# Kernel optimization log

Measured on AMD Instinct MI355X. Metric: run time of the kernel, lower is better.

## Reference

```python
import jax, jax.numpy as jnp
import numpy as np

B, S, D = 4, 2048, 1024
NEG_INF = jnp.float32(-jnp.inf)


def setup_inputs() -> dict:
    key = jax.random.key(0)
    kx, kq, kk, kv = jax.random.split(key, 4)
    scale = 0.02
    return {
        "x": jax.random.normal(kx, (B, S, D), dtype=jnp.float32),
        "Wq": jax.random.normal(kq, (D, D), dtype=jnp.float32) * scale,
        "Wk": jax.random.normal(kk, (D, D), dtype=jnp.float32) * scale,
        "Wv": jax.random.normal(kv, (D, D), dtype=jnp.float32) * scale,
    }


def reference(x, Wq, Wk, Wv):
    # nn.Linear(d_in, d_out): y = x @ W.T (no bias; qkv_bias=False)
    q = jnp.einsum("bsd,ed->bse", x, Wq)
    k = jnp.einsum("bsd,ed->bse", x, Wk)
    v = jnp.einsum("bsd,ed->bse", x, Wv)
    n = x.shape[1]
    scores = jnp.einsum("bqe,bke->bqk", q, k)  # [B, S, S]
    # causal mask: positions k > q are masked with -inf
    causal = jnp.tril(jnp.ones((n, n), dtype=bool))
    scores = jnp.where(causal[None, :, :], scores, NEG_INF)
    attn = jax.nn.softmax(scores / jnp.sqrt(jnp.float32(k.shape[-1])), axis=-1)
    # dropout p=0.0 (eval) -> identity
    return jnp.einsum("bqk,bke->bqe", attn, v)
```

## Files before the change

kernel.cpp:

```cpp
#include <hip/hip_runtime.h>
#include <hip/hip_bf16.h>
#include <stdint.h>
#include <stddef.h>


typedef __hip_bfloat16 bf16;
typedef short short8 __attribute__((ext_vector_type(8)));
typedef short short4v __attribute__((ext_vector_type(4)));
typedef float f32x4 __attribute__((ext_vector_type(4)));

#define BM 128
#define BN 128
#define BK 64
#define MSZ 8192
#define DD 1024

__device__ __forceinline__ void cstore(float* p, float v) { *p = v; }
__device__ __forceinline__ void cstore(bf16* p, float v) { *p = __float2bfloat16(v); }

__global__ __launch_bounds__(256)
void f2b(const float* __restrict__ s, bf16* __restrict__ d, int n) {
  const int i = (blockIdx.x * 256 + threadIdx.x) * 4;
  if (i >= n) return;
  const float4 v = *(const float4*)(s + i);
  bf16 t[4] = {__float2bfloat16(v.x), __float2bfloat16(v.y),
               __float2bfloat16(v.z), __float2bfloat16(v.w)};
  *(short4v*)(d + i) = *(short4v*)t;
}

__global__ __launch_bounds__(256)
void f2b3(const float* __restrict__ a, const float* __restrict__ b,
          const float* __restrict__ c, bf16* __restrict__ d, int n) {
  const float* s = (blockIdx.y == 0) ? a : (blockIdx.y == 1) ? b : c;
  const int i = (blockIdx.x * 256 + threadIdx.x) * 4;
  if (i >= n) return;
  const float4 v = *(const float4*)(s + i);
  bf16 t[4] = {__float2bfloat16(v.x), __float2bfloat16(v.y),
               __float2bfloat16(v.z), __float2bfloat16(v.w)};
  *(short4v*)(d + (size_t)blockIdx.y * n + i) = *(short4v*)t;
}

template <int MODE, typename CT>
__global__ __launch_bounds__(256, 3)
void gemm_bt(const bf16* __restrict__ A, const bf16* __restrict__ B,
             CT* __restrict__ C, bf16* __restrict__ C2,
             int lda, int ldb, int ldc, int K,
             long sA, long sB, long sC, float scale) {
  int by, bx;
  if (MODE == 2) {
    const int t = blockIdx.x;
    by = (int)((__fsqrt_rn(8.f * (float)t + 1.f) - 1.f) * 0.5f);
    while ((by + 1) * (by + 2) / 2 <= t) by++;
    while (by * (by + 1) / 2 > t) by--;
    bx = t - by * (by + 1) / 2;
  } else if (MODE == 3) {
    by = gridDim.y - 1 - blockIdx.y;
    bx = blockIdx.x;
  } else {
    by = blockIdx.y;
    bx = blockIdx.x;
  }

  __shared__ short8 As[8 * 128];
  __shared__ short8 Bs[8 * 128];

  const int tid = threadIdx.x;
  const int wave = tid >> 6, lane = tid & 63;
  const int wm = wave >> 1, wn = wave & 1;
  const int l15 = lane & 15, q4 = lane >> 4;
  const int bm0 = by * BM, bn0 = bx * BN;

  const bf16* Az = A + (long)blockIdx.z * sA;
  const bf16* Bz = B + (long)blockIdx.z * sB;
  CT* Cz = C + (long)blockIdx.z * sC;

  const int kg = (lane >> 3) & 7;
  const int rl = wave * 8 + (lane & 7);

  const bf16* apg = Az + (size_t)(bm0 + rl) * lda + kg * 8;
  const bf16* bpg = Bz + (size_t)(bn0 + rl) * ldb + kg * 8;
  const size_t la32 = (size_t)32 * lda, lb32 = (size_t)32 * ldb;
  short8* dstA = &As[kg * 128 + rl];
  short8* dstB = &Bs[kg * 128 + rl];

  const int Ke = (MODE == 3) ? min(K, (by + 1) * BM) : K;

  f32x4 acc[4][4] = {};
  short8 ra[4], rb[4];

#pragma unroll
  for (int j = 0; j < 4; j++) {
    ra[j] = *(const short8*)(apg + j * la32);
    rb[j] = *(const short8*)(bpg + j * lb32);
  }

  for (int k0 = 0; k0 < Ke; k0 += BK) {
    __syncthreads();
#pragma unroll
    for (int j = 0; j < 4; j++) {
      dstA[j * 32] = ra[j];
      dstB[j * 32] = rb[j];
    }
    __syncthreads();

    const int kn = k0 + BK;
    if (kn < Ke) {
#pragma unroll
      for (int j = 0; j < 4; j++) {
        ra[j] = *(const short8*)(apg + j * la32 + kn);
        rb[j] = *(const short8*)(bpg + j * lb32 + kn);
      }
    }

#pragma unroll
    for (int s = 0; s < 2; s++) {
      const int ch = (s * 4 + q4) * 128;
      short8 af[4], bfr[4];
#pragma unroll
      for (int i = 0; i < 4; i++)
        af[i] = As[ch + wm * 64 + i * 16 + l15];
#pragma unroll
      for (int j = 0; j < 4; j++)
        bfr[j] = Bs[ch + wn * 64 + j * 16 + l15];
#pragma unroll
      for (int i = 0; i < 4; i++)
#pragma unroll
        for (int j = 0; j < 4; j++)
          acc[i][j] = __builtin_amdgcn_mfma_f32_16x16x32_bf16(af[i], bfr[j], acc[i][j], 0, 0, 0);
    }
  }

  if (MODE == 1 && bx >= 16) {
#pragma unroll
    for (int i = 0; i < 4; i++) {
#pragma unroll
      for (int j = 0; j < 4; j++) {
        const int rowb = bm0 + wm * 64 + i * 16 + q4 * 4;
        const int v = (bn0 - 2048) + wn * 64 + j * 16 + l15;
        bf16 t[4] = {__float2bfloat16(acc[i][j][0]), __float2bfloat16(acc[i][j][1]),
                     __float2bfloat16(acc[i][j][2]), __float2bfloat16(acc[i][j][3])};
        *(short4v*)(C2 + (size_t)v * MSZ + rowb) = *(short4v*)t;
      }
    }
    return;
  }

  CT* Cb = Cz;
  int coff = bn0;
  if (MODE == 1) {
    Cb = Cz + (bx >= 8 ? (size_t)MSZ * DD : 0);
    coff = (bx & 7) * BN;
  }
#pragma unroll
  for (int i = 0; i < 4; i++) {
#pragma unroll
    for (int j = 0; j < 4; j++) {
#pragma unroll
      for (int r = 0; r < 4; r++) {
        const int row = bm0 + wm * 64 + i * 16 + q4 * 4 + r;
        const int col = coff + wn * 64 + j * 16 + l15;
        cstore(&Cb[(size_t)row * ldc + col], acc[i][j][r] * scale);
      }
    }
  }
}

__global__ __launch_bounds__(256)
void softmax_rows(const bf16* __restrict__ Sc, bf16* __restrict__ P, int S) {
  const int q = blockIdx.x, b = blockIdx.y;
  const short8* srow = (const short8*)(Sc + ((size_t)b * S + q) * S);
  short8* prow = (short8*)(P + ((size_t)b * S + q) * S);
  const int len = q + 1;
  const int tid = threadIdx.x;
  const int wave = tid >> 6, lane = tid & 63;
  __shared__ float red[10];

  const short8 raw = srow[tid];
  float v[8];
#pragma unroll
  for (int j = 0; j < 8; j++) {
    const int k = tid * 8 + j;
    const float f = __bfloat162float(((const bf16*)&raw)[j]);
    v[j] = (k < len) ? f : -1e30f;
  }

  float m = v[0];
#pragma unroll
  for (int j = 1; j < 8; j++) m = fmaxf(m, v[j]);
#pragma unroll
  for (int o = 32; o; o >>= 1) m = fmaxf(m, __shfl_down(m, o));
  if (lane == 0) red[wave] = m;
  __syncthreads();
  if (tid == 0) red[8] = fmaxf(fmaxf(red[0], red[1]), fmaxf(red[2], red[3]));
  __syncthreads();
  const float M = red[8];

  float e[8], s = 0.f;
#pragma unroll
  for (int j = 0; j < 8; j++) { e[j] = __expf(v[j] - M); s += e[j]; }
#pragma unroll
  for (int o = 32; o; o >>= 1) s += __shfl_down(s, o);
  if (lane == 0) red[4 + wave] = s;
  __syncthreads();
  if (tid == 0) red[9] = red[4] + red[5] + red[6] + red[7];
  __syncthreads();
  const float inv = 1.f / red[9];

  short8 outp;
#pragma unroll
  for (int j = 0; j < 8; j++) {
    const int k = tid * 8 + j;
    ((bf16*)&outp)[j] = __float2bfloat16((k < len) ? e[j] * inv : 0.f);
  }
  prow[tid] = outp;
}

extern "C" void kernel_launch(void* const* d_in, const int* in_sizes, int n_in,
                              void* d_out, int out_size, void* d_ws, size_t ws_size,
                              hipStream_t stream) {
  const float* x  = (const float*)d_in[0];
  const float* Wq = (const float*)d_in[1];
  const float* Wk = (const float*)d_in[2];
  const float* Wv = (const float*)d_in[3];
  float* out = (float*)d_out;

  const int Bb = 4, S = 2048, D = 1024, MS = Bb * S;

  char* ws = (char*)d_ws;
  bf16* xb = (bf16*)ws;
  bf16* wb = (bf16*)(ws + (size_t)MS * D * 2);
  bf16* Q  = (bf16*)(ws + (size_t)MS * D * 2 + 3u * D * D * 2);
  bf16* Kp = Q + (size_t)MS * D;
  bf16* VT = Kp + (size_t)MS * D;
  bf16* Sc = VT + (size_t)MS * D;
  bf16* P  = (bf16*)ws;
  (void)Kp;

  dim3 blk(256);

  f2b<<<dim3(MS * D / 4 / 256), blk, 0, stream>>>(x, xb, MS * D);
  f2b3<<<dim3(D * D / 4 / 256, 3), blk, 0, stream>>>(Wq, Wk, Wv, wb, D * D);

  gemm_bt<1, bf16><<<dim3(3 * D / BN, MS / BM, 1), blk, 0, stream>>>(
      xb, wb, Q, VT, D, D, D, D, 0, 0, 0, 1.f);
  gemm_bt<2, bf16><<<dim3(136, 1, Bb), blk, 0, stream>>>(
      Q, Kp, Sc, nullptr, D, D, S, D,
      (long)S * D, (long)S * D, (long)S * S, 0.03125f);
  softmax_rows<<<dim3(S, Bb), blk, 0, stream>>>(Sc, P, S);
  gemm_bt<3, float><<<dim3(D / BN, S / BM, Bb), blk, 0, stream>>>(
      P, VT, out, nullptr, S, MS, D, S,
      (long)S * S, (long)S, (long)S * D, 1.f);
}
```

Baseline: 314.1 us.

## Fuse softmax exp and row sums into score GEMM, normalize in PV epilogue

Removes the standalone softmax kernel. The score GEMM epilogue now applies the causal mask, computes exp of the scaled scores without subtracting the row max, writes unnormalized probabilities and atomically accumulates row sums. The PV GEMM divides by the row sum in its epilogue. The QKV projection also moves to a dedicated 256x128-tile kernel with 512 threads. This saves a full read and write pass over the score matrix, but skipping the max subtraction risks overflow for larger score magnitudes, and it adds a zeroing launch plus atomics.

```diff
diff --git a/kernel.cpp b/kernel.cpp
--- a/kernel.cpp
+++ b/kernel.cpp
@@ -9,14 +9,15 @@
 typedef short short4v __attribute__((ext_vector_type(4)));
 typedef float f32x4 __attribute__((ext_vector_type(4)));
 
-#define BM 128
-#define BN 128
-#define BK 64
+#define S2 2048
+#define DD 1024
 #define MSZ 8192
-#define DD 1024
-
-__device__ __forceinline__ void cstore(float* p, float v) { *p = v; }
-__device__ __forceinline__ void cstore(bf16* p, float v) { *p = __float2bfloat16(v); }
+
+__global__ __launch_bounds__(256)
+void zerok(float* __restrict__ p, int n) {
+  const int i = blockIdx.x * 256 + threadIdx.x;
+  if (i < n) p[i] = 0.f;
+}
 
 __global__ __launch_bounds__(256)
 void f2b(const float* __restrict__ s, bf16* __restrict__ d, int n) {
@@ -40,88 +41,53 @@
   *(short4v*)(d + (size_t)blockIdx.y * n + i) = *(short4v*)t;
 }
 
-template <int MODE, typename CT>
-__global__ __launch_bounds__(256, 3)
-void gemm_bt(const bf16* __restrict__ A, const bf16* __restrict__ B,
-             CT* __restrict__ C, bf16* __restrict__ C2,
-             int lda, int ldb, int ldc, int K,
-             long sA, long sB, long sC, float scale) {
-  int by, bx;
-  if (MODE == 2) {
-    const int t = blockIdx.x;
-    by = (int)((__fsqrt_rn(8.f * (float)t + 1.f) - 1.f) * 0.5f);
-    while ((by + 1) * (by + 2) / 2 <= t) by++;
-    while (by * (by + 1) / 2 > t) by--;
-    bx = t - by * (by + 1) / 2;
-  } else if (MODE == 3) {
-    by = gridDim.y - 1 - blockIdx.y;
-    bx = blockIdx.x;
-  } else {
-    by = blockIdx.y;
-    bx = blockIdx.x;
-  }
-
-  __shared__ short8 As[8 * 128];
+__global__ __launch_bounds__(512, 6)
+void gemm_qkv(const bf16* __restrict__ A, const bf16* __restrict__ B,
+              bf16* __restrict__ Cq, bf16* __restrict__ Vt) {
+  const int bx = blockIdx.x, by = blockIdx.y;
+  __shared__ short8 As[8 * 256];
   __shared__ short8 Bs[8 * 128];
-
-  const int tid = threadIdx.x;
-  const int wave = tid >> 6, lane = tid & 63;
+  const int tid = threadIdx.x, wave = tid >> 6, lane = tid & 63;
   const int wm = wave >> 1, wn = wave & 1;
   const int l15 = lane & 15, q4 = lane >> 4;
-  const int bm0 = by * BM, bn0 = bx * BN;
-
-  const bf16* Az = A + (long)blockIdx.z * sA;
-  const bf16* Bz = B + (long)blockIdx.z * sB;
-  CT* Cz = C + (long)blockIdx.z * sC;
-
-  const int kg = (lane >> 3) & 7;
-  const int rl = wave * 8 + (lane & 7);
-
-  const bf16* apg = Az + (size_t)(bm0 + rl) * lda + kg * 8;
-  const bf16* bpg = Bz + (size_t)(bn0 + rl) * ldb + kg * 8;
-  const size_t la32 = (size_t)32 * lda, lb32 = (size_t)32 * ldb;
-  short8* dstA = &As[kg * 128 + rl];
+  const int bm0 = by * 256, bn0 = bx * 128;
+  const int kg = (lane >> 3) & 7, rl = wave * 8 + (lane & 7);
+
+  const bf16* apg = A + (size_t)(bm0 + rl) * DD + kg * 8;
+  const bf16* bpg = B + (size_t)(bn0 + rl) * DD + kg * 8;
+  short8* dstA = &As[kg * 256 + rl];
   short8* dstB = &Bs[kg * 128 + rl];
-
-  const int Ke = (MODE == 3) ? min(K, (by + 1) * BM) : K;
+  const size_t l64 = (size_t)64 * DD;
 
   f32x4 acc[4][4] = {};
-  short8 ra[4], rb[4];
-
-#pragma unroll
-  for (int j = 0; j < 4; j++) {
-    ra[j] = *(const short8*)(apg + j * la32);
-    rb[j] = *(const short8*)(bpg + j * lb32);
-  }
-
-  for (int k0 = 0; k0 < Ke; k0 += BK) {
-    __syncthreads();
-#pragma unroll
-    for (int j = 0; j < 4; j++) {
-      dstA[j * 32] = ra[j];
-      dstB[j * 32] = rb[j];
-    }
-    __syncthreads();
-
-    const int kn = k0 + BK;
-    if (kn < Ke) {
-#pragma unroll
-      for (int j = 0; j < 4; j++) {
-        ra[j] = *(const short8*)(apg + j * la32 + kn);
-        rb[j] = *(const short8*)(bpg + j * lb32 + kn);
-      }
-    }
-
+  short8 ra[4], rb[2];
+#pragma unroll
+  for (int j = 0; j < 4; j++) ra[j] = *(const short8*)(apg + j * l64);
+#pragma unroll
+  for (int j = 0; j < 2; j++) rb[j] = *(const short8*)(bpg + j * l64);
+
+  for (int k0 = 0; k0 < DD; k0 += 64) {
+    __syncthreads();
+#pragma unroll
+    for (int j = 0; j < 4; j++) dstA[j * 64] = ra[j];
+#pragma unroll
+    for (int j = 0; j < 2; j++) dstB[j * 64] = rb[j];
+    __syncthreads();
+    const int kn = k0 + 64;
+    if (kn < DD) {
+#pragma unroll
+      for (int j = 0; j < 4; j++) ra[j] = *(const short8*)(apg + j * l64 + kn);
+#pragma unroll
+      for (int j = 0; j < 2; j++) rb[j] = *(const short8*)(bpg + j * l64 + kn);
+    }
 #pragma unroll
     for (int s = 0; s < 2; s++) {
-      const int ch = (s * 4 + q4) * 128;
+      const int ch = s * 4 + q4;
       short8 af[4], bfr[4];
 #pragma unroll
-      for (int i = 0; i < 4; i++)
-        af[i] = As[ch + wm * 64 + i * 16 + l15];
-#pragma unroll
-      for (int j = 0; j < 4; j++)
-        bfr[j] = Bs[ch + wn * 64 + j * 16 + l15];
+      for (int i = 0; i < 4; i++) af[i] = As[ch * 256 + wm * 64 + i * 16 + l15];
+#pragma unroll
+      for (int j = 0; j < 4; j++) bfr[j] = Bs[ch * 128 + wn * 64 + j * 16 + l15];
 #pragma unroll
       for (int i = 0; i < 4; i++)
 #pragma unroll
@@ -130,89 +96,195 @@
     }
   }
 
-  if (MODE == 1 && bx >= 16) {
-#pragma unroll
-    for (int i = 0; i < 4; i++) {
+  if (bx >= 16) {
+#pragma unroll
+    for (int i = 0; i < 4; i++)
 #pragma unroll
       for (int j = 0; j < 4; j++) {
         const int rowb = bm0 + wm * 64 + i * 16 + q4 * 4;
         const int v = (bn0 - 2048) + wn * 64 + j * 16 + l15;
         bf16 t[4] = {__float2bfloat16(acc[i][j][0]), __float2bfloat16(acc[i][j][1]),
                      __float2bfloat16(acc[i][j][2]), __float2bfloat16(acc[i][j][3])};
-        *(short4v*)(C2 + (size_t)v * MSZ + rowb) = *(short4v*)t;
-      }
-    }
+        *(short4v*)(Vt + (size_t)v * MSZ + rowb) = *(short4v*)t;
+      }
     return;
   }
-
-  CT* Cb = Cz;
-  int coff = bn0;
-  if (MODE == 1) {
-    Cb = Cz + (bx >= 8 ? (size_t)MSZ * DD : 0);
-    coff = (bx & 7) * BN;
-  }
-#pragma unroll
-  for (int i = 0; i < 4; i++) {
-#pragma unroll
-    for (int j = 0; j < 4; j++) {
+  bf16* Cb = Cq + (bx >= 8 ? (size_t)MSZ * DD : 0);
+  const int coff = (bx & 7) * 128;
+#pragma unroll
+  for (int i = 0; i < 4; i++)
+#pragma unroll
+    for (int j = 0; j < 4; j++)
 #pragma unroll
       for (int r = 0; r < 4; r++) {
         const int row = bm0 + wm * 64 + i * 16 + q4 * 4 + r;
         const int col = coff + wn * 64 + j * 16 + l15;
-        cstore(&Cb[(size_t)row * ldc + col], acc[i][j][r] * scale);
-      }
-    }
-  }
-}
-
-__global__ __launch_bounds__(256)
-void softmax_rows(const bf16* __restrict__ Sc, bf16* __restrict__ P, int S) {
-  const int q = blockIdx.x, b = blockIdx.y;
-  const short8* srow = (const short8*)(Sc + ((size_t)b * S + q) * S);
-  short8* prow = (short8*)(P + ((size_t)b * S + q) * S);
-  const int len = q + 1;
-  const int tid = threadIdx.x;
-  const int wave = tid >> 6, lane = tid & 63;
-  __shared__ float red[10];
-
-  const short8 raw = srow[tid];
-  float v[8];
-#pragma unroll
-  for (int j = 0; j < 8; j++) {
-    const int k = tid * 8 + j;
-    const float f = __bfloat162float(((const bf16*)&raw)[j]);
-    v[j] = (k < len) ? f : -1e30f;
-  }
-
-  float m = v[0];
-#pragma unroll
-  for (int j = 1; j < 8; j++) m = fmaxf(m, v[j]);
-#pragma unroll
-  for (int o = 32; o; o >>= 1) m = fmaxf(m, __shfl_down(m, o));
-  if (lane == 0) red[wave] = m;
-  __syncthreads();
-  if (tid == 0) red[8] = fmaxf(fmaxf(red[0], red[1]), fmaxf(red[2], red[3]));
-  __syncthreads();
-  const float M = red[8];
-
-  float e[8], s = 0.f;
-#pragma unroll
-  for (int j = 0; j < 8; j++) { e[j] = __expf(v[j] - M); s += e[j]; }
-#pragma unroll
-  for (int o = 32; o; o >>= 1) s += __shfl_down(s, o);
-  if (lane == 0) red[4 + wave] = s;
-  __syncthreads();
-  if (tid == 0) red[9] = red[4] + red[5] + red[6] + red[7];
-  __syncthreads();
-  const float inv = 1.f / red[9];
-
-  short8 outp;
-#pragma unroll
-  for (int j = 0; j < 8; j++) {
-    const int k = tid * 8 + j;
-    ((bf16*)&outp)[j] = __float2bfloat16((k < len) ? e[j] * inv : 0.f);
-  }
-  prow[tid] = outp;
+        Cb[(size_t)row * DD + col] = __float2bfloat16(acc[i][j][r]);
+      }
+}
+
+__global__ __launch_bounds__(256, 3)
+void gemm_sc(const bf16* __restrict__ Qm, const bf16* __restrict__ Km,
+             bf16* __restrict__ Sc, float* __restrict__ rowsum) {
+  const int t = blockIdx.x;
+  int by = (int)((__fsqrt_rn(8.f * (float)t + 1.f) - 1.f) * 0.5f);
+  while ((by + 1) * (by + 2) / 2 <= t) by++;
+  while (by * (by + 1) / 2 > t) by--;
+  const int bx = t - by * (by + 1) / 2;
+  const int z = blockIdx.z;
+
+  __shared__ short8 As[8 * 128];
+  __shared__ short8 Bs[8 * 128];
+  const int tid = threadIdx.x, wave = tid >> 6, lane = tid & 63;
+  const int wm = wave >> 1, wn = wave & 1;
+  const int l15 = lane & 15, q4 = lane >> 4;
+  const int bm0 = by * 128, bn0 = bx * 128;
+
+  const bf16* Az = Qm + (size_t)z * S2 * DD;
+  const bf16* Bz = Km + (size_t)z * S2 * DD;
+  bf16* Cz = Sc + (size_t)z * S2 * S2;
+
+  const int kg = (lane >> 3) & 7, rl = wave * 8 + (lane & 7);
+  const bf16* apg = Az + (size_t)(bm0 + rl) * DD + kg * 8;
+  const bf16* bpg = Bz + (size_t)(bn0 + rl) * DD + kg * 8;
+  const size_t l32 = (size_t)32 * DD;
+  short8* dstA = &As[kg * 128 + rl];
+  short8* dstB = &Bs[kg * 128 + rl];
+
+  f32x4 acc[4][4] = {};
+  short8 ra[4], rb[4];
+#pragma unroll
+  for (int j = 0; j < 4; j++) {
+    ra[j] = *(const short8*)(apg + j * l32);
+    rb[j] = *(const short8*)(bpg + j * l32);
+  }
+  for (int k0 = 0; k0 < DD; k0 += 64) {
+    __syncthreads();
+#pragma unroll
+    for (int j = 0; j < 4; j++) { dstA[j * 32] = ra[j]; dstB[j * 32] = rb[j]; }
+    __syncthreads();
+    const int kn = k0 + 64;
+    if (kn < DD) {
+#pragma unroll
+      for (int j = 0; j < 4; j++) {
+        ra[j] = *(const short8*)(apg + j * l32 + kn);
+        rb[j] = *(const short8*)(bpg + j * l32 + kn);
+      }
+    }
+#pragma unroll
+    for (int s = 0; s < 2; s++) {
+      const int ch = (s * 4 + q4) * 128;
+      short8 af[4], bfr[4];
+#pragma unroll
+      for (int i = 0; i < 4; i++) af[i] = As[ch + wm * 64 + i * 16 + l15];
+#pragma unroll
+      for (int j = 0; j < 4; j++) bfr[j] = Bs[ch + wn * 64 + j * 16 + l15];
+#pragma unroll
+      for (int i = 0; i < 4; i++)
+#pragma unroll
+        for (int j = 0; j < 4; j++)
+          acc[i][j] = __builtin_amdgcn_mfma_f32_16x16x32_bf16(af[i], bfr[j], acc[i][j], 0, 0, 0);
+    }
+  }
+
+#pragma unroll
+  for (int i = 0; i < 4; i++) {
+#pragma unroll
+    for (int r = 0; r < 4; r++) {
+      const int row = bm0 + wm * 64 + i * 16 + q4 * 4 + r;
+      float rsum = 0.f;
+#pragma unroll
+      for (int j = 0; j < 4; j++) {
+        const int col = bn0 + wn * 64 + j * 16 + l15;
+        const float p = (col <= row) ? __expf(acc[i][j][r] * 0.03125f) : 0.f;
+        Cz[(size_t)row * S2 + col] = __float2bfloat16(p);
+        rsum += p;
+      }
+      rsum += __shfl_xor(rsum, 1);
+      rsum += __shfl_xor(rsum, 2);
+      rsum += __shfl_xor(rsum, 4);
+      rsum += __shfl_xor(rsum, 8);
+      if (l15 == 0) atomicAdd(&rowsum[z * S2 + row], rsum);
+    }
+  }
+}
+
+__global__ __launch_bounds__(256, 3)
+void gemm_pv(const bf16* __restrict__ Pm, const bf16* __restrict__ Vt,
+             float* __restrict__ O, const float* __restrict__ rowsum) {
+  const int bx = blockIdx.x;
+  const int by = gridDim.y - 1 - blockIdx.y;
+  const int z = blockIdx.z;
+
+  __shared__ short8 As[8 * 128];
+  __shared__ short8 Bs[8 * 128];
+  const int tid = threadIdx.x, wave = tid >> 6, lane = tid & 63;
+  const int wm = wave >> 1, wn = wave & 1;
+  const int l15 = lane & 15, q4 = lane >> 4;
+  const int bm0 = by * 128, bn0 = bx * 128;
+
+  const bf16* Az = Pm + (size_t)z * S2 * S2;
+  const bf16* Bz = Vt + (size_t)z * S2;
+  float* Cz = O + (size_t)z * S2 * DD;
+
+  const int kg = (lane >> 3) & 7, rl = wave * 8 + (lane & 7);
+  const bf16* apg = Az + (size_t)(bm0 + rl) * S2 + kg * 8;
+  const bf16* bpg = Bz + (size_t)(bn0 + rl) * MSZ + kg * 8;
+  const size_t la32 = (size_t)32 * S2, lb32 = (size_t)32 * MSZ;
+  short8* dstA = &As[kg * 128 + rl];
+  short8* dstB = &Bs[kg * 128 + rl];
+
+  const int Ke = (by + 1) * 128;
+
+  f32x4 acc[4][4] = {};
+  short8 ra[4], rb[4];
+#pragma unroll
+  for (int j = 0; j < 4; j++) {
+    ra[j] = *(const short8*)(apg + j * la32);
+    rb[j] = *(const short8*)(bpg + j * lb32);
+  }
+  for (int k0 = 0; k0 < Ke; k0 += 64) {
+    __syncthreads();
+#pragma unroll
+    for (int j = 0; j < 4; j++) { dstA[j * 32] = ra[j]; dstB[j * 32] = rb[j]; }
+    __syncthreads();
+    const int kn = k0 + 64;
+    if (kn < Ke) {
+#pragma unroll
+      for (int j = 0; j < 4; j++) {
+        ra[j] = *(const short8*)(apg + j * la32 + kn);
+        rb[j] = *(const short8*)(bpg + j * lb32 + kn);
+      }
+    }
+#pragma unroll
+    for (int s = 0; s < 2; s++) {
+      const int ch = (s * 4 + q4) * 128;
+      short8 af[4], bfr[4];
+#pragma unroll
+      for (int i = 0; i < 4; i++) af[i] = As[ch + wm * 64 + i * 16 + l15];
+#pragma unroll
+      for (int j = 0; j < 4; j++) bfr[j] = Bs[ch + wn * 64 + j * 16 + l15];
+#pragma unroll
+      for (int i = 0; i < 4; i++)
+#pragma unroll
+        for (int j = 0; j < 4; j++)
+          acc[i][j] = __builtin_amdgcn_mfma_f32_16x16x32_bf16(af[i], bfr[j], acc[i][j], 0, 0, 0);
+    }
+  }
+
+#pragma unroll
+  for (int i = 0; i < 4; i++) {
+#pragma unroll
+    for (int r = 0; r < 4; r++) {
+      const int row = bm0 + wm * 64 + i * 16 + q4 * 4 + r;
+      const float inv = 1.f / rowsum[z * S2 + row];
+#pragma unroll
+      for (int j = 0; j < 4; j++) {
+        const int col = bn0 + wn * 64 + j * 16 + l15;
+        Cz[(size_t)row * DD + col] = acc[i][j][r] * inv;
+      }
+    }
+  }
 }
 
 extern "C" void kernel_launch(void* const* d_in, const int* in_sizes, int n_in,
@@ -227,27 +299,21 @@
   const int Bb = 4, S = 2048, D = 1024, MS = Bb * S;
 
   char* ws = (char*)d_ws;
-  bf16* xb = (bf16*)ws;
-  bf16* wb = (bf16*)(ws + (size_t)MS * D * 2);
-  bf16* Q  = (bf16*)(ws + (size_t)MS * D * 2 + 3u * D * D * 2);
-  bf16* Kp = Q + (size_t)MS * D;
-  bf16* VT = Kp + (size_t)MS * D;
-  bf16* Sc = VT + (size_t)MS * D;
-  bf16* P  = (bf16*)ws;
-  (void)Kp;
+  bf16*  xb = (bf16*)ws;
+  bf16*  wb = (bf16*)(ws + (size_t)MS * D * 2);
+  bf16*  Q  = (bf16*)(ws + (size_t)MS * D * 2 + 3u * D * D * 2);
+  bf16*  Kp = Q + (size_t)MS * D;
+  bf16*  VT = Kp + (size_t)MS * D;
+  bf16*  Sc = VT + (size_t)MS * D;
+  float* rowsum = (float*)(Sc + (size_t)Bb * S * S);
 
   dim3 blk(256);
 
+  zerok<<<dim3(MS / 256), blk, 0, stream>>>(rowsum, MS);
   f2b<<<dim3(MS * D / 4 / 256), blk, 0, stream>>>(x, xb, MS * D);
   f2b3<<<dim3(D * D / 4 / 256, 3), blk, 0, stream>>>(Wq, Wk, Wv, wb, D * D);
 
-  gemm_bt<1, bf16><<<dim3(3 * D / BN, MS / BM, 1), blk, 0, stream>>>(
-      xb, wb, Q, VT, D, D, D, D, 0, 0, 0, 1.f);
-  gemm_bt<2, bf16><<<dim3(136, 1, Bb), blk, 0, stream>>>(
-      Q, Kp, Sc, nullptr, D, D, S, D,
-      (long)S * D, (long)S * D, (long)S * S, 0.03125f);
-  softmax_rows<<<dim3(S, Bb), blk, 0, stream>>>(Sc, P, S);
-  gemm_bt<3, float><<<dim3(D / BN, S / BM, Bb), blk, 0, stream>>>(
-      P, VT, out, nullptr, S, MS, D, S,
-      (long)S * S, (long)S, (long)S * D, 1.f);
-}
+  gemm_qkv<<<dim3(3 * D / 128, MS / 256), dim3(512), 0, stream>>>(xb, wb, Q, VT);
+  gemm_sc<<<dim3(136, 1, Bb), blk, 0, stream>>>(Q, Kp, Sc, rowsum);
+  gemm_pv<<<dim3(D / 128, S / 128, Bb), blk, 0, stream>>>(Sc, VT, out, rowsum);
+}
```

Measured after the change: 606.3 us. +93.0%, slower.
